# Optimization experiments

Measured on AMD Instinct MI355X. Metric: run time of the kernel, lower is better.

The kernel has to match this reference:

```python
import jax, jax.numpy as jnp
import numpy as np

NUM_MODES = 192
LAYERS = [NUM_MODES * 2, 256, 128, 32]


def setup_inputs() -> dict:
    key = jax.random.key(0)
    ks = jax.random.split(key, 7)
    B, C, L = 64, 512, 1024
    x = jax.random.normal(ks[0], (B, C, L), dtype=jnp.float32)
    params = {}
    for i in range(3):
        fan_in, fan_out = LAYERS[i], LAYERS[i + 1]
        bound = 1.0 / np.sqrt(fan_in)
        params[f"W{i+1}"] = jax.random.uniform(ks[1 + 2 * i], (fan_in, fan_out), dtype=jnp.float32, minval=-bound, maxval=bound)
        params[f"b{i+1}"] = jax.random.uniform(ks[2 + 2 * i], (fan_out,), dtype=jnp.float32, minval=-bound, maxval=bound)
    return {"x": x, **params}


def reference(x, W1, b1, W2, b2, W3, b3):
    # rfft over last dim -> complex [B, C, L//2+1]
    f = jnp.fft.rfft(x, axis=-1)
    # view_as_real + slice first NUM_MODES bins -> [B, C, NUM_MODES, 2] (real, imag interleaved)
    f = f[..., :NUM_MODES]
    feat = jnp.stack([f.real, f.imag], axis=-1).reshape(*x.shape[:-1], NUM_MODES * 2)
    h = jax.nn.leaky_relu(feat @ W1 + b1, negative_slope=0.01)
    h = jax.nn.leaky_relu(h @ W2 + b2, negative_slope=0.01)
    return h @ W3 + b3
```

## Files before the change

### kernel.cpp

```cpp
#include <hip/hip_runtime.h>

typedef __attribute__((ext_vector_type(8))) short short8;
typedef __attribute__((ext_vector_type(4))) float f32x4;

__device__ __forceinline__ unsigned short f2bf(float f) {
  unsigned int u = __float_as_uint(f);
  u += 0x7fffu + ((u >> 16) & 1u);
  return (unsigned short)(u >> 16);
}

__device__ __forceinline__ short8 load_af(const unsigned short* p) {
  union { uint2 u[2]; short8 v; } r;
  r.u[0] = *(const uint2*)(p);
  r.u[1] = *(const uint2*)(p + 16);
  return r.v;
}

__global__ void prep_dw1_kernel(const float* __restrict__ W1, float* __restrict__ dw1) {
  __shared__ float cs[1536];
  __shared__ float sn[1536];
  const int t = threadIdx.x;
  const int n0 = blockIdx.x * 8;
  for (int i = t; i < 1536; i += 256) {
    int r = i / 192, m = i - r * 192;
    int ph = ((n0 + r) * m) & 1023;
    float ang = (float)ph * 6.135923151542565e-3f;
    float s, c;
    __sincosf(ang, &s, &c);
    cs[i] = c;
    sn[i] = s;
  }
  __syncthreads();
  float acc[8] = {0.f, 0.f, 0.f, 0.f, 0.f, 0.f, 0.f, 0.f};
  for (int m = 0; m < 192; ++m) {
    float wre = W1[(2 * m) * 256 + t];
    float wim = W1[(2 * m + 1) * 256 + t];
#pragma unroll
    for (int r = 0; r < 8; ++r) {
      acc[r] += cs[r * 192 + m] * wre - sn[r * 192 + m] * wim;
    }
  }
#pragma unroll
  for (int r = 0; r < 8; ++r) dw1[(size_t)(n0 + r) * 256 + t] = acc[r];
}

__global__ void prep_swz_kernel(const float* __restrict__ W2, const float* __restrict__ W3,
                                const float* __restrict__ dw1,
                                unsigned short* __restrict__ fL1,
                                unsigned short* __restrict__ fL2,
                                unsigned short* __restrict__ fL3) {
  int g = blockIdx.x * 256 + threadIdx.x;
  int tile = g >> 6, lane = g & 63;
  const float* src;
  unsigned short* dst;
  int ldN, KS, tl;
  if (tile < 512)      { tl = tile;       src = dw1; dst = fL1; ldN = 256; KS = 32; }
  else if (tile < 576) { tl = tile - 512; src = W2;  dst = fL2; ldN = 128; KS = 8; }
  else                 { tl = tile - 576; src = W3;  dst = fL3; ldN = 32;  KS = 4; }
  int nt = tl / KS, kk = tl - nt * KS;
  int k0 = kk * 32 + ((lane >> 4) << 2);
  int col = nt * 16 + (lane & 15);
  unsigned int d[4];
#pragma unroll
  for (int dw = 0; dw < 4; ++dw) {
    int e0 = dw * 2, e1 = e0 + 1;
    int ka = k0 + (e0 & 3) + ((e0 >> 2) << 4);
    int kb = k0 + (e1 & 3) + ((e1 >> 2) << 4);
    d[dw] = (unsigned int)f2bf(src[ka * ldN + col]) |
            ((unsigned int)f2bf(src[kb * ldN + col]) << 16);
  }
  uint4 v; v.x = d[0]; v.y = d[1]; v.z = d[2]; v.w = d[3];
  *(uint4*)(dst + ((size_t)tl * 64 + lane) * 8) = v;
}

#define XS_S 136
#define H1_S 264
#define H2_S 136

__global__ __launch_bounds__(256, 2) void mlp_kernel(
    const float* __restrict__ x,
    const float* __restrict__ b1, const float* __restrict__ b2,
    const float* __restrict__ b3,
    const unsigned short* __restrict__ fL1, const unsigned short* __restrict__ fL2,
    const unsigned short* __restrict__ fL3, float* __restrict__ out) {
  __shared__ unsigned short xs[64 * XS_S];
  __shared__ unsigned short hs1[64 * H1_S];
  __shared__ unsigned short hs2[64 * H2_S];
  const int t = threadIdx.x;
  const int lane = t & 63;
  const int wid = t >> 6;
  const int rlo = lane & 15;
  const int g4 = (lane >> 4) << 2;
  const size_t row0 = (size_t)blockIdx.x * 64;

  f32x4 acc[4][4] = {};

  for (int kc = 0; kc < 8; ++kc) {
#pragma unroll
    for (int i = 0; i < 8; ++i) {
      int idx = i * 256 + t;
      int row = idx >> 5, cg = idx & 31;
      const float4* p = (const float4*)(x + (row0 + row) * 1024 + kc * 128 + cg * 4);
      float4 v = *p;
      uint2 w;
      w.x = (unsigned int)f2bf(v.x) | ((unsigned int)f2bf(v.y) << 16);
      w.y = (unsigned int)f2bf(v.z) | ((unsigned int)f2bf(v.w) << 16);
      *(uint2*)(xs + row * XS_S + cg * 4) = w;
    }
    __syncthreads();
#pragma unroll
    for (int ks = 0; ks < 4; ++ks) {
      short8 af[4];
#pragma unroll
      for (int m = 0; m < 4; ++m)
        af[m] = load_af(xs + (m * 16 + rlo) * XS_S + ks * 32 + g4);
      short8 bfr[4];
#pragma unroll
      for (int c = 0; c < 4; ++c)
        bfr[c] = *(const short8*)(fL1 +
                 (((size_t)(wid * 4 + c) * 32 + kc * 4 + ks) * 64 + lane) * 8);
#pragma unroll
      for (int m = 0; m < 4; ++m)
#pragma unroll
        for (int c = 0; c < 4; ++c)
          acc[m][c] = __builtin_amdgcn_mfma_f32_16x16x32_bf16(af[m], bfr[c], acc[m][c], 0, 0, 0);
    }
    __syncthreads();
  }

  {
    float bv[4];
#pragma unroll
    for (int c = 0; c < 4; ++c) bv[c] = b1[wid * 64 + c * 16 + rlo];
#pragma unroll
    for (int m = 0; m < 4; ++m)
#pragma unroll
      for (int c = 0; c < 4; ++c)
#pragma unroll
        for (int r = 0; r < 4; ++r) {
          float v = acc[m][c][r] + bv[c];
          v = fmaxf(v, 0.01f * v);
          hs1[(m * 16 + g4 + r) * H1_S + wid * 64 + c * 16 + rlo] = f2bf(v);
        }
  }
  __syncthreads();

  f32x4 a2[4][2] = {};
#pragma unroll
  for (int ks = 0; ks < 8; ++ks) {
    short8 af[4];
#pragma unroll
    for (int m = 0; m < 4; ++m)
      af[m] = load_af(hs1 + (m * 16 + rlo) * H1_S + ks * 32 + g4);
    short8 bfr[2];
#pragma unroll
    for (int c = 0; c < 2; ++c)
      bfr[c] = *(const short8*)(fL2 + (((size_t)(wid * 2 + c) * 8 + ks) * 64 + lane) * 8);
#pragma unroll
    for (int m = 0; m < 4; ++m)
#pragma unroll
      for (int c = 0; c < 2; ++c)
        a2[m][c] = __builtin_amdgcn_mfma_f32_16x16x32_bf16(af[m], bfr[c], a2[m][c], 0, 0, 0);
  }
  {
    float bv[2];
#pragma unroll
    for (int c = 0; c < 2; ++c) bv[c] = b2[wid * 32 + c * 16 + rlo];
#pragma unroll
    for (int m = 0; m < 4; ++m)
#pragma unroll
      for (int c = 0; c < 2; ++c)
#pragma unroll
        for (int r = 0; r < 4; ++r) {
          float v = a2[m][c][r] + bv[c];
          v = fmaxf(v, 0.01f * v);
          hs2[(m * 16 + g4 + r) * H2_S + wid * 32 + c * 16 + rlo] = f2bf(v);
        }
  }
  __syncthreads();

  f32x4 a3[2] = {};
#pragma unroll
  for (int ks = 0; ks < 4; ++ks) {
    short8 af = load_af(hs2 + (wid * 16 + rlo) * H2_S + ks * 32 + g4);
#pragma unroll
    for (int c = 0; c < 2; ++c) {
      short8 bfr = *(const short8*)(fL3 + (((size_t)c * 4 + ks) * 64 + lane) * 8);
      a3[c] = __builtin_amdgcn_mfma_f32_16x16x32_bf16(af, bfr, a3[c], 0, 0, 0);
    }
  }
  {
    float bv[2];
    bv[0] = b3[rlo];
    bv[1] = b3[16 + rlo];
#pragma unroll
    for (int c = 0; c < 2; ++c)
#pragma unroll
      for (int r = 0; r < 4; ++r)
        out[(row0 + wid * 16 + g4 + r) * 32 + c * 16 + rlo] = a3[c][r] + bv[c];
  }
}

extern "C" void kernel_launch(void* const* d_in, const int* in_sizes, int n_in,
                              void* d_out, int out_size, void* d_ws, size_t ws_size,
                              hipStream_t stream) {
  const float* x  = (const float*)d_in[0];
  const float* W1 = (const float*)d_in[1];
  const float* b1 = (const float*)d_in[2];
  const float* W2 = (const float*)d_in[3];
  const float* b2 = (const float*)d_in[4];
  const float* W3 = (const float*)d_in[5];
  const float* b3 = (const float*)d_in[6];
  float* out = (float*)d_out;

  char* ws = (char*)d_ws;
  float* dw1          = (float*)ws;
  unsigned short* fL1 = (unsigned short*)(ws + 1048576);
  unsigned short* fL2 = (unsigned short*)(ws + 1572864);
  unsigned short* fL3 = (unsigned short*)(ws + 1638400);

  hipLaunchKernelGGL(prep_dw1_kernel, dim3(128), dim3(256), 0, stream, W1, dw1);
  hipLaunchKernelGGL(prep_swz_kernel, dim3(146), dim3(256), 0, stream, W2, W3, dw1,
                     fL1, fL2, fL3);
  hipLaunchKernelGGL(mlp_kernel, dim3(512), dim3(256), 0, stream,
                     x, b1, b2, b3, fL1, fL2, fL3, out);
}
```

Baseline: 261.5 us.

## Fuse weight prep into one kernel and double-buffer x tiles in MLP

Merges the DFT-folded W1 computation and swizzle into a single prep kernel. It uses a rotation recurrence instead of a sincos table and writes bf16 fragments directly, which removes one launch and the fp32 dw1 round trip. The main kernel now register-prefetches the next x chunk and the next B fragments, and double-buffers the LDS x tile so one barrier per chunk is dropped. It also unions the LDS buffers with h1/h2, shrinks padding, and raises launch bounds to three blocks per SM. The recurrence can accumulate rounding error over 192 steps, and the extra register staging may pressure the occupancy target.

```diff
diff --git a/kernel.cpp b/kernel.cpp
--- a/kernel.cpp
+++ b/kernel.cpp
@@ -1,13 +1,8 @@
 #include <hip/hip_runtime.h>
+#include <hip/hip_bf16.h>
 
 typedef __attribute__((ext_vector_type(8))) short short8;
 typedef __attribute__((ext_vector_type(4))) float f32x4;
-
-__device__ __forceinline__ unsigned short f2bf(float f) {
-  unsigned int u = __float_as_uint(f);
-  u += 0x7fffu + ((u >> 16) & 1u);
-  return (unsigned short)(u >> 16);
-}
 
 __device__ __forceinline__ short8 load_af(const unsigned short* p) {
   union { uint2 u[2]; short8 v; } r;
@@ -16,117 +11,182 @@
   return r.v;
 }
 
-__global__ void prep_dw1_kernel(const float* __restrict__ W1, float* __restrict__ dw1) {
-  __shared__ float cs[1536];
-  __shared__ float sn[1536];
-  const int t = threadIdx.x;
-  const int n0 = blockIdx.x * 8;
-  for (int i = t; i < 1536; i += 256) {
-    int r = i / 192, m = i - r * 192;
-    int ph = ((n0 + r) * m) & 1023;
-    float ang = (float)ph * 6.135923151542565e-3f;
-    float s, c;
-    __sincosf(ang, &s, &c);
-    cs[i] = c;
-    sn[i] = s;
-  }
-  __syncthreads();
-  float acc[8] = {0.f, 0.f, 0.f, 0.f, 0.f, 0.f, 0.f, 0.f};
-  for (int m = 0; m < 192; ++m) {
-    float wre = W1[(2 * m) * 256 + t];
-    float wim = W1[(2 * m + 1) * 256 + t];
-#pragma unroll
-    for (int r = 0; r < 8; ++r) {
-      acc[r] += cs[r * 192 + m] * wre - sn[r * 192 + m] * wim;
-    }
-  }
-#pragma unroll
-  for (int r = 0; r < 8; ++r) dw1[(size_t)(n0 + r) * 256 + t] = acc[r];
-}
-
-__global__ void prep_swz_kernel(const float* __restrict__ W2, const float* __restrict__ W3,
-                                const float* __restrict__ dw1,
-                                unsigned short* __restrict__ fL1,
-                                unsigned short* __restrict__ fL2,
-                                unsigned short* __restrict__ fL3) {
-  int g = blockIdx.x * 256 + threadIdx.x;
-  int tile = g >> 6, lane = g & 63;
-  const float* src;
-  unsigned short* dst;
-  int ldN, KS, tl;
-  if (tile < 512)      { tl = tile;       src = dw1; dst = fL1; ldN = 256; KS = 32; }
-  else if (tile < 576) { tl = tile - 512; src = W2;  dst = fL2; ldN = 128; KS = 8; }
-  else                 { tl = tile - 576; src = W3;  dst = fL3; ldN = 32;  KS = 4; }
-  int nt = tl / KS, kk = tl - nt * KS;
-  int k0 = kk * 32 + ((lane >> 4) << 2);
-  int col = nt * 16 + (lane & 15);
-  unsigned int d[4];
-#pragma unroll
-  for (int dw = 0; dw < 4; ++dw) {
-    int e0 = dw * 2, e1 = e0 + 1;
-    int ka = k0 + (e0 & 3) + ((e0 >> 2) << 4);
-    int kb = k0 + (e1 & 3) + ((e1 >> 2) << 4);
-    d[dw] = (unsigned int)f2bf(src[ka * ldN + col]) |
-            ((unsigned int)f2bf(src[kb * ldN + col]) << 16);
-  }
-  uint4 v; v.x = d[0]; v.y = d[1]; v.z = d[2]; v.w = d[3];
-  *(uint4*)(dst + ((size_t)tl * 64 + lane) * 8) = v;
-}
-
-#define XS_S 136
-#define H1_S 264
-#define H2_S 136
-
-__global__ __launch_bounds__(256, 2) void mlp_kernel(
+__device__ __forceinline__ unsigned int pk_bf16(float a, float b) {
+  __hip_bfloat162 h = __float22bfloat162_rn(make_float2(a, b));
+  return *(unsigned int*)&h;
+}
+__device__ __forceinline__ unsigned short s_bf16(float a) {
+  __hip_bfloat16 h = __float2bfloat16(a);
+  return *(unsigned short*)&h;
+}
+
+__global__ __launch_bounds__(256) void prep_kernel(
+    const float* __restrict__ W1, const float* __restrict__ W2,
+    const float* __restrict__ W3,
+    unsigned short* __restrict__ fL1, unsigned short* __restrict__ fL2,
+    unsigned short* __restrict__ fL3) {
+  const int w = blockIdx.x * 4 + (threadIdx.x >> 6);
+  const int lane = threadIdx.x & 63;
+  const int rlo = lane & 15;
+  const int q4 = (lane >> 4) << 2;
+
+  if (w < 512) {
+    const int nt = w >> 5, kk = w & 31;
+    const int col = nt * 16 + rlo;
+    const int k0 = kk * 32 + q4;
+    float pc[8], ps[8], dc[8], dsn[8], acc[8];
+#pragma unroll
+    for (int e = 0; e < 8; ++e) {
+      int ke = k0 + (e & 3) + ((e >> 2) << 4);
+      float ang = (float)ke * 6.135923151542565e-3f;
+      float s, c;
+      __sincosf(ang, &s, &c);
+      dc[e] = c; dsn[e] = s;
+      pc[e] = 1.f; ps[e] = 0.f;
+      acc[e] = 0.f;
+    }
+    const float* pw = W1 + col;
+#pragma unroll 2
+    for (int m = 0; m < 192; ++m) {
+      float wre = pw[0];
+      float wio = pw[256];
+      pw += 512;
+#pragma unroll
+      for (int e = 0; e < 8; ++e) {
+        acc[e] = fmaf(pc[e], wre, acc[e]);
+        acc[e] = fmaf(-ps[e], wio, acc[e]);
+        float c2 = pc[e] * dc[e] - ps[e] * dsn[e];
+        float s2 = ps[e] * dc[e] + pc[e] * dsn[e];
+        pc[e] = c2; ps[e] = s2;
+      }
+    }
+    uint4 v;
+    v.x = pk_bf16(acc[0], acc[1]);
+    v.y = pk_bf16(acc[2], acc[3]);
+    v.z = pk_bf16(acc[4], acc[5]);
+    v.w = pk_bf16(acc[6], acc[7]);
+    *(uint4*)(fL1 + ((size_t)w * 64 + lane) * 8) = v;
+  } else if (w < 576) {
+    const int tl = w - 512;
+    const int nt = tl >> 3, kk = tl & 7;
+    const int col = nt * 16 + rlo;
+    const int k0 = kk * 32 + q4;
+    float a[8];
+#pragma unroll
+    for (int e = 0; e < 8; ++e) {
+      int ke = k0 + (e & 3) + ((e >> 2) << 4);
+      a[e] = W2[ke * 128 + col];
+    }
+    uint4 v;
+    v.x = pk_bf16(a[0], a[1]); v.y = pk_bf16(a[2], a[3]);
+    v.z = pk_bf16(a[4], a[5]); v.w = pk_bf16(a[6], a[7]);
+    *(uint4*)(fL2 + ((size_t)tl * 64 + lane) * 8) = v;
+  } else {
+    const int tl = w - 576;
+    const int nt = tl >> 2, kk = tl & 3;
+    const int col = nt * 16 + rlo;
+    const int k0 = kk * 32 + q4;
+    float a[8];
+#pragma unroll
+    for (int e = 0; e < 8; ++e) {
+      int ke = k0 + (e & 3) + ((e >> 2) << 4);
+      a[e] = W3[ke * 32 + col];
+    }
+    uint4 v;
+    v.x = pk_bf16(a[0], a[1]); v.y = pk_bf16(a[2], a[3]);
+    v.z = pk_bf16(a[4], a[5]); v.w = pk_bf16(a[6], a[7]);
+    *(uint4*)(fL3 + ((size_t)tl * 64 + lane) * 8) = v;
+  }
+}
+
+#define XS_S 132
+#define H1_S 260
+#define H2_S 132
+
+struct P2 {
+  unsigned short h1[64 * H1_S];
+  unsigned short h2[64 * H2_S];
+};
+union SH {
+  unsigned short xs[2][64 * XS_S];
+  P2 p2;
+};
+
+__global__ __launch_bounds__(256, 3) void mlp_kernel(
     const float* __restrict__ x,
     const float* __restrict__ b1, const float* __restrict__ b2,
     const float* __restrict__ b3,
     const unsigned short* __restrict__ fL1, const unsigned short* __restrict__ fL2,
     const unsigned short* __restrict__ fL3, float* __restrict__ out) {
-  __shared__ unsigned short xs[64 * XS_S];
-  __shared__ unsigned short hs1[64 * H1_S];
-  __shared__ unsigned short hs2[64 * H2_S];
+  __shared__ SH sh;
   const int t = threadIdx.x;
   const int lane = t & 63;
   const int wid = t >> 6;
   const int rlo = lane & 15;
   const int g4 = (lane >> 4) << 2;
   const size_t row0 = (size_t)blockIdx.x * 64;
+  const float* xb = x + row0 * 1024;
 
   f32x4 acc[4][4] = {};
 
+  float4 st[8];
+#pragma unroll
+  for (int i = 0; i < 8; ++i) {
+    int idx = i * 256 + t;
+    int row = idx >> 5, cg = idx & 31;
+    st[i] = *(const float4*)(xb + row * 1024 + cg * 4);
+  }
+
   for (int kc = 0; kc < 8; ++kc) {
+    unsigned short* xbuf = sh.xs[kc & 1];
 #pragma unroll
     for (int i = 0; i < 8; ++i) {
       int idx = i * 256 + t;
       int row = idx >> 5, cg = idx & 31;
-      const float4* p = (const float4*)(x + (row0 + row) * 1024 + kc * 128 + cg * 4);
-      float4 v = *p;
-      uint2 w;
-      w.x = (unsigned int)f2bf(v.x) | ((unsigned int)f2bf(v.y) << 16);
-      w.y = (unsigned int)f2bf(v.z) | ((unsigned int)f2bf(v.w) << 16);
-      *(uint2*)(xs + row * XS_S + cg * 4) = w;
-    }
+      uint2 wv;
+      wv.x = pk_bf16(st[i].x, st[i].y);
+      wv.y = pk_bf16(st[i].z, st[i].w);
+      *(uint2*)(xbuf + row * XS_S + cg * 4) = wv;
+    }
+    if (kc < 7) {
+#pragma unroll
+      for (int i = 0; i < 8; ++i) {
+        int idx = i * 256 + t;
+        int row = idx >> 5, cg = idx & 31;
+        st[i] = *(const float4*)(xb + row * 1024 + (kc + 1) * 128 + cg * 4);
+      }
+    }
+    short8 bcur[4];
+#pragma unroll
+    for (int c = 0; c < 4; ++c)
+      bcur[c] = *(const short8*)(fL1 +
+                (((size_t)(wid * 4 + c) * 32 + kc * 4) * 64 + lane) * 8);
     __syncthreads();
 #pragma unroll
     for (int ks = 0; ks < 4; ++ks) {
+      short8 bnext[4];
+      if (ks < 3) {
+#pragma unroll
+        for (int c = 0; c < 4; ++c)
+          bnext[c] = *(const short8*)(fL1 +
+                    (((size_t)(wid * 4 + c) * 32 + kc * 4 + ks + 1) * 64 + lane) * 8);
+      }
       short8 af[4];
 #pragma unroll
       for (int m = 0; m < 4; ++m)
-        af[m] = load_af(xs + (m * 16 + rlo) * XS_S + ks * 32 + g4);
-      short8 bfr[4];
-#pragma unroll
-      for (int c = 0; c < 4; ++c)
-        bfr[c] = *(const short8*)(fL1 +
-                 (((size_t)(wid * 4 + c) * 32 + kc * 4 + ks) * 64 + lane) * 8);
+        af[m] = load_af(xbuf + (m * 16 + rlo) * XS_S + ks * 32 + g4);
 #pragma unroll
       for (int m = 0; m < 4; ++m)
 #pragma unroll
         for (int c = 0; c < 4; ++c)
-          acc[m][c] = __builtin_amdgcn_mfma_f32_16x16x32_bf16(af[m], bfr[c], acc[m][c], 0, 0, 0);
-    }
-    __syncthreads();
-  }
+          acc[m][c] = __builtin_amdgcn_mfma_f32_16x16x32_bf16(af[m], bcur[c], acc[m][c], 0, 0, 0);
+      if (ks < 3) {
+#pragma unroll
+        for (int c = 0; c < 4; ++c) bcur[c] = bnext[c];
+      }
+    }
+  }
+  __syncthreads();
 
   {
     float bv[4];
@@ -140,7 +200,7 @@
         for (int r = 0; r < 4; ++r) {
           float v = acc[m][c][r] + bv[c];
           v = fmaxf(v, 0.01f * v);
-          hs1[(m * 16 + g4 + r) * H1_S + wid * 64 + c * 16 + rlo] = f2bf(v);
+          sh.p2.h1[(m * 16 + g4 + r) * H1_S + wid * 64 + c * 16 + rlo] = s_bf16(v);
         }
   }
   __syncthreads();
@@ -151,7 +211,7 @@
     short8 af[4];
 #pragma unroll
     for (int m = 0; m < 4; ++m)
-      af[m] = load_af(hs1 + (m * 16 + rlo) * H1_S + ks * 32 + g4);
+      af[m] = load_af(sh.p2.h1 + (m * 16 + rlo) * H1_S + ks * 32 + g4);
     short8 bfr[2];
 #pragma unroll
     for (int c = 0; c < 2; ++c)
@@ -174,7 +234,7 @@
         for (int r = 0; r < 4; ++r) {
           float v = a2[m][c][r] + bv[c];
           v = fmaxf(v, 0.01f * v);
-          hs2[(m * 16 + g4 + r) * H2_S + wid * 32 + c * 16 + rlo] = f2bf(v);
+          sh.p2.h2[(m * 16 + g4 + r) * H2_S + wid * 32 + c * 16 + rlo] = s_bf16(v);
         }
   }
   __syncthreads();
@@ -182,7 +242,7 @@
   f32x4 a3[2] = {};
 #pragma unroll
   for (int ks = 0; ks < 4; ++ks) {
-    short8 af = load_af(hs2 + (wid * 16 + rlo) * H2_S + ks * 32 + g4);
+    short8 af = load_af(sh.p2.h2 + (wid * 16 + rlo) * H2_S + ks * 32 + g4);
 #pragma unroll
     for (int c = 0; c < 2; ++c) {
       short8 bfr = *(const short8*)(fL3 + (((size_t)c * 4 + ks) * 64 + lane) * 8);
@@ -214,14 +274,12 @@
   float* out = (float*)d_out;
 
   char* ws = (char*)d_ws;
-  float* dw1          = (float*)ws;
-  unsigned short* fL1 = (unsigned short*)(ws + 1048576);
-  unsigned short* fL2 = (unsigned short*)(ws + 1572864);
-  unsigned short* fL3 = (unsigned short*)(ws + 1638400);
-
-  hipLaunchKernelGGL(prep_dw1_kernel, dim3(128), dim3(256), 0, stream, W1, dw1);
-  hipLaunchKernelGGL(prep_swz_kernel, dim3(146), dim3(256), 0, stream, W2, W3, dw1,
-                     fL1, fL2, fL3);
+  unsigned short* fL1 = (unsigned short*)ws;
+  unsigned short* fL2 = (unsigned short*)(ws + 524288);
+  unsigned short* fL3 = (unsigned short*)(ws + 589824);
+
+  hipLaunchKernelGGL(prep_kernel, dim3(146), dim3(256), 0, stream,
+                     W1, W2, W3, fL1, fL2, fL3);
   hipLaunchKernelGGL(mlp_kernel, dim3(512), dim3(256), 0, stream,
                      x, b1, b2, b3, fL1, fL2, fL3, out);
 }
```

Result: slower. 291.2 us (+11.3%).
